# Kernel tuning notes

Measured on AMD Instinct MI355X. Metric: run time of the kernel, lower is better.

Reference implementation:

```python
import jax, jax.numpy as jnp
import numpy as np

N0, N1, N2 = 100000, 20000, 4000   # nodes per hierarchy level
F, H, C = 128, 128, 10             # num_features, hidden_dim, num_classes
E0, E1, E2 = 1600000, 320000, 64000  # intra-level edges (avg degree 16)
EPS = 1e-5                          # BatchNorm eps


def setup_inputs() -> dict:
    key = jax.random.key(0)
    ks = jax.random.split(key, 16)
    s = 0.05
    return {
        "x": jax.random.normal(ks[0], (N0, F), jnp.float32),
        "ei0": jax.random.randint(ks[1], (2, E0), 0, N0),
        "ei1": jax.random.randint(ks[2], (2, E1), 0, N1),
        "ei2": jax.random.randint(ks[3], (2, E2), 0, N2),
        "parent1": jax.random.randint(ks[4], (N0,), 0, N1),
        "parent2": jax.random.randint(ks[5], (N1,), 0, N2),
        "W0": jax.random.normal(ks[6], (F, H), jnp.float32) * s,
        "b0": jnp.zeros((H,), jnp.float32),
        "W1": jax.random.normal(ks[7], (H, H), jnp.float32) * s,
        "b1": jnp.zeros((H,), jnp.float32),
        "W2": jax.random.normal(ks[8], (H, H), jnp.float32) * s,
        "b2": jnp.zeros((H,), jnp.float32),
        "W3": jax.random.normal(ks[9], (2 * H, H), jnp.float32) * s,
        "b3": jnp.zeros((H,), jnp.float32),
        "W4": jax.random.normal(ks[10], (2 * H, C), jnp.float32) * s,
        "b4": jnp.zeros((C,), jnp.float32),
        "pW": jax.random.normal(ks[11], (4, H, H), jnp.float32) * s,
        "pb": jnp.zeros((4, H), jnp.float32),
        "pgamma": jnp.ones((4, H), jnp.float32),
        "pbeta": jnp.zeros((4, H), jnp.float32),
        "pmean": jax.random.normal(ks[12], (4, H), jnp.float32) * 0.1,
        "pvar": jax.random.uniform(ks[13], (4, H), jnp.float32, 0.5, 1.5),
    }


def _gcn(x, ei, W, b):
    # GCNConv: add self loops, symmetric D^-1/2 (A+I) D^-1/2 normalization.
    n = x.shape[0]
    loops = jnp.arange(n)
    row = jnp.concatenate([ei[0], loops])  # source nodes
    col = jnp.concatenate([ei[1], loops])  # target nodes
    deg = jax.ops.segment_sum(jnp.ones(row.shape, x.dtype), col, num_segments=n)
    dis = deg ** -0.5  # deg >= 1 because of self loops
    norm = dis[row] * dis[col]
    xw = x @ W
    out = jax.ops.segment_sum(norm[:, None] * xw[row], col, num_segments=n)
    return out + b


def _pool_nn(y, W, b, g, beta, mean, var):
    # SEPooling nn: Linear -> ReLU -> BatchNorm1d (eval mode, running stats)
    y = jax.nn.relu(y @ W + b)
    return (y - mean) * (g / jnp.sqrt(var + EPS)) + beta


def reference(x, ei0, ei1, ei2, parent1, parent2,
              W0, b0, W1, b1, W2, b2, W3, b3, W4, b4,
              pW, pb, pgamma, pbeta, pmean, pvar):
    relu = jax.nn.relu
    # down path (dropout is identity in eval mode)
    h0 = relu(_gcn(x, ei0, W0, b0))  # [N0,H]; stored skip xs[0]
    p = jax.ops.segment_sum(h0, parent1, num_segments=N1)  # scatter-add children -> parents
    x1 = relu(_pool_nn(p, pW[0], pb[0], pgamma[0], pbeta[0], pmean[0], pvar[0]))
    h1 = relu(_gcn(x1, ei1, W1, b1))  # [N1,H]; stored skip xs[1]
    p = jax.ops.segment_sum(h1, parent2, num_segments=N2)
    x2 = relu(_pool_nn(p, pW[1], pb[1], pgamma[1], pbeta[1], pmean[1], pvar[1]))
    # up path: conv, unpool (gather parent feature per child), concat skip
    h = relu(_gcn(x2, ei2, W2, b2))  # [N2,H]
    xu = relu(_pool_nn(h[parent2], pW[2], pb[2], pgamma[2], pbeta[2], pmean[2], pvar[2]))  # [N1,H]
    xc = jnp.concatenate([xu, h1], axis=1)  # [N1,2H]
    h = relu(_gcn(xc, ei1, W3, b3))  # [N1,H]
    xu = relu(_pool_nn(h[parent1], pW[3], pb[3], pgamma[3], pbeta[3], pmean[3], pvar[3]))  # [N0,H]
    xc = jnp.concatenate([xu, h0], axis=1)  # [N0,2H]
    out = _gcn(xc, ei0, W4, b4)  # [N0,C]
    return jax.nn.log_softmax(out, axis=-1)
```

## Files before the change

kernel.cpp:

```cpp
#include <hip/hip_runtime.h>
#include <math.h>

#define N0 100000
#define N1 20000
#define N2 4000
#define HDIM 128
#define E0C 1600000
#define E1C 320000
#define E2C 64000
#define EPSBN 1e-5f

typedef unsigned int u32;
typedef float f32x4 __attribute__((ext_vector_type(4)));
typedef short bf16x8 __attribute__((ext_vector_type(8)));

union FragU { uint4 u; bf16x8 h; };
__device__ __forceinline__ bf16x8 asbf(uint4 v) { FragU x; x.u = v; return x.h; }

__device__ __forceinline__ float bl(u32 p) { return __uint_as_float(p << 16); }
__device__ __forceinline__ float bh(u32 p) { return __uint_as_float(p & 0xFFFF0000u); }
__device__ __forceinline__ u32 pack2(float a, float b) {
    u32 ua = __float_as_uint(a), ub = __float_as_uint(b);
    ua = (ua + 0x7FFFu + ((ua >> 16) & 1u)) >> 16;
    ub = (ub + 0x7FFFu + ((ub >> 16) & 1u)) >> 16;
    return ua | (ub << 16);
}

#define OFF0 0
#define OFF1 (N0)
#define OFF2 (N0 + N1)
#define OFF3 (N0 + N1 + N2)
#define OFF4 (N0 + N1 + N2 + N1)
#define OFFT (N0 + N1 + N2 + N1 + N2)

#define S0 (E0C)
#define S1 (E0C + E1C)
#define S2 (E0C + E1C + E2C)
#define S3 (E0C + E1C + E2C + N0)
#define S4 (E0C + E1C + E2C + N0 + N1)

#define NBUCK ((OFFT + 1023) / 1024)
#define ITEMS_PER_BLK 2048
#define NBA ((S4 + ITEMS_PER_BLK - 1) / ITEMS_PER_BLK)
#define BH_N (NBUCK * NBA)
#define NBLK2 ((BH_N + 1023) / 1024)

#define NWMAT 9


__device__ __forceinline__ void item_full(int g,
    const int* __restrict__ ei0r, const int* __restrict__ ei0c,
    const int* __restrict__ ei1r, const int* __restrict__ ei1c,
    const int* __restrict__ ei2r, const int* __restrict__ ei2c,
    const int* __restrict__ p1, const int* __restrict__ p2,
    int& concat, int& payload)
{
    if (g < S0)      { concat = ei0c[g];             payload = ei0r[g]; }
    else if (g < S1) { int i = g - S0; concat = OFF1 + ei1c[i]; payload = ei1r[i]; }
    else if (g < S2) { int i = g - S1; concat = OFF2 + ei2c[i]; payload = ei2r[i]; }
    else if (g < S3) { int i = g - S2; concat = OFF3 + p1[i];   payload = i; }
    else             { int i = g - S3; concat = OFF4 + p2[i];   payload = i; }
}

__device__ __forceinline__ int item_concat(int g,
    const int* __restrict__ ei0c, const int* __restrict__ ei1c, const int* __restrict__ ei2c,
    const int* __restrict__ p1, const int* __restrict__ p2)
{
    if (g < S0)      return ei0c[g];
    else if (g < S1) return OFF1 + ei1c[g - S0];
    else if (g < S2) return OFF2 + ei2c[g - S1];
    else if (g < S3) return OFF3 + p1[g - S2];
    else             return OFF4 + p2[g - S3];
}

__global__ __launch_bounds__(256) void binhist_kernel(
    const int* __restrict__ ei0c, const int* __restrict__ ei1c, const int* __restrict__ ei2c,
    const int* __restrict__ p1, const int* __restrict__ p2,
    int* __restrict__ blockHist,
    const float* __restrict__ W0p, const float* __restrict__ W1p,
    const float* __restrict__ W2p, const float* __restrict__ W3p,
    const float* __restrict__ pWp, u32* __restrict__ Wpk)
{
    __shared__ int hist[NBUCK];
    int tid = threadIdx.x, blk = blockIdx.x;
    if (blk >= NBA) {
        int b = blk - NBA;
        const float* src;
        if (b == 0) src = W0p;
        else if (b == 1) src = W1p;
        else if (b == 2) src = W2p;
        else if (b == 3) src = W3p;
        else if (b == 4) src = W3p + 128 * 128;
        else src = pWp + (b - 5) * 128 * 128;
        u32* dst = Wpk + b * 8192;
        #pragma unroll
        for (int it = 0; it < 32; it++) {
            int flat = it * 256 + tid;
            int i = flat & 3;
            int ln = (flat >> 2) & 63;
            int s = (flat >> 8) & 3;
            int t = flat >> 10;
            int mm = ln & 15, qq = ln >> 4;
            int k0 = s * 32 + qq * 8 + 2 * i;
            int col = t * 16 + mm;
            dst[flat] = pack2(src[k0 * 128 + col], src[(k0 + 1) * 128 + col]);
        }
        return;
    }
    for (int i = tid; i < NBUCK; i += 256) hist[i] = 0;
    __syncthreads();
    int base = blk * ITEMS_PER_BLK;
    #pragma unroll
    for (int k = 0; k < ITEMS_PER_BLK / 256; k++) {
        int g = base + k * 256 + tid;
        if (g < S4) {
            int c = item_concat(g, ei0c, ei1c, ei2c, p1, p2);
            atomicAdd(&hist[c >> 10], 1);
        }
    }
    __syncthreads();
    for (int b = tid; b < NBUCK; b += 256) blockHist[b * NBA + blk] = hist[b];
}

__global__ __launch_bounds__(256) void scan_k1(const int* __restrict__ c, int* __restrict__ bsum, int n) {
    int t = threadIdx.x;
    int base = blockIdx.x * 1024 + t * 4;
    int s = 0;
    #pragma unroll
    for (int j = 0; j < 4; j++) {
        int idx = base + j;
        if (idx < n) s += c[idx];
    }
    #pragma unroll
    for (int o = 32; o > 0; o >>= 1) s += __shfl_down(s, o, 64);
    __shared__ int ws[4];
    if ((t & 63) == 0) ws[t >> 6] = s;
    __syncthreads();
    if (t == 0) bsum[blockIdx.x] = ws[0] + ws[1] + ws[2] + ws[3];
}

__global__ __launch_bounds__(256) void scan_k2(int* __restrict__ bsum, int* __restrict__ totalOut, int nb,
    const float* __restrict__ g, const float* __restrict__ beta,
    const float* __restrict__ mean, const float* __restrict__ var,
    float* __restrict__ scale, float* __restrict__ shift)
{
    int t = threadIdx.x;
    #pragma unroll
    for (int j = 0; j < 2; j++) {
        int i = j * 256 + t;
        float s = g[i] * rsqrtf(var[i] + EPSBN);
        scale[i] = s;
        shift[i] = beta[i] - mean[i] * s;
    }
    int v = (t < nb) ? bsum[t] : 0;
    __shared__ int ts[256];
    ts[t] = v;
    __syncthreads();
    for (int o = 1; o < 256; o <<= 1) {
        int u = (t >= o) ? ts[t - o] : 0;
        __syncthreads();
        ts[t] += u;
        __syncthreads();
    }
    if (t < nb) bsum[t] = ts[t] - v;
    if (t == nb - 1) *totalOut = ts[t];
}

__global__ __launch_bounds__(256) void scan_k3(const int* __restrict__ c, const int* __restrict__ bsum,
                                               const int* __restrict__ total,
                                               int* __restrict__ S, int n) {
    int t = threadIdx.x;
    int base = blockIdx.x * 1024 + t * 4;
    int v[4];
    #pragma unroll
    for (int j = 0; j < 4; j++) v[j] = (base + j < n) ? c[base + j] : 0;
    int tsum = v[0] + v[1] + v[2] + v[3];
    __shared__ int ts[256];
    ts[t] = tsum;
    __syncthreads();
    for (int o = 1; o < 256; o <<= 1) {
        int u = (t >= o) ? ts[t - o] : 0;
        __syncthreads();
        ts[t] += u;
        __syncthreads();
    }
    int run = bsum[blockIdx.x] + ts[t] - tsum;
    #pragma unroll
    for (int j = 0; j < 4; j++) {
        if (base + j < n) { S[base + j] = run; run += v[j]; }
    }
    if (blockIdx.x == 0 && t == 0) S[n] = *total;
}

__global__ __launch_bounds__(256) void binfill_kernel(
    const int* __restrict__ ei0r, const int* __restrict__ ei0c,
    const int* __restrict__ ei1r, const int* __restrict__ ei1c,
    const int* __restrict__ ei2r, const int* __restrict__ ei2c,
    const int* __restrict__ p1, const int* __restrict__ p2,
    const int* __restrict__ OfsAbs, u32* __restrict__ binPair)
{
    __shared__ int cur[NBUCK];
    int tid = threadIdx.x, blk = blockIdx.x;
    for (int i = tid; i < NBUCK; i += 256) cur[i] = OfsAbs[i * NBA + blk];
    __syncthreads();
    int base = blk * ITEMS_PER_BLK;
    #pragma unroll
    for (int k = 0; k < ITEMS_PER_BLK / 256; k++) {
        int g = base + k * 256 + tid;
        if (g < S4) {
            int c, p;
            item_full(g, ei0r, ei0c, ei1r, ei1c, ei2r, ei2c, p1, p2, c, p);
            int pos = atomicAdd(&cur[c >> 10], 1);
            binPair[pos] = ((u32)(c & 1023) << 17) | (u32)p;
        }
    }
}

__global__ __launch_bounds__(1024) void bucket_build_kernel(
    const u32* __restrict__ binPair, const int* __restrict__ OfsAbs,
    int* __restrict__ rpAll, int* __restrict__ srcU,
    float* __restrict__ dis0, float* __restrict__ dis1, float* __restrict__ dis2)
{
    __shared__ int cnt_l[1024];
    __shared__ int rp_l[1024];
    __shared__ int wsum[16];
    int b = blockIdx.x, tid = threadIdx.x;
    int start = OfsAbs[b * NBA];
    int end = (b + 1 < NBUCK) ? OfsAbs[(b + 1) * NBA] : S4;
    int d0 = b << 10;
    int nd = OFFT - d0; if (nd > 1024) nd = 1024;

    cnt_l[tid] = 0;
    __syncthreads();
    for (int i = start + tid; i < end; i += 1024) {
        u32 e = binPair[i];
        atomicAdd(&cnt_l[e >> 17], 1);
    }
    __syncthreads();
    int v = cnt_l[tid];
    int lane = tid & 63, wv = tid >> 6;
    int s = v;
    #pragma unroll
    for (int o = 1; o < 64; o <<= 1) {
        int u = __shfl_up(s, o, 64);
        if (lane >= o) s += u;
    }
    if (lane == 63) wsum[wv] = s;
    __syncthreads();
    if (wv == 0) {
        int t2 = (lane < 16) ? wsum[lane] : 0;
        #pragma unroll
        for (int o = 1; o < 16; o <<= 1) {
            int u = __shfl_up(t2, o, 64);
            if (lane >= o) t2 += u;
        }
        if (lane < 16) wsum[lane] = t2;
    }
    __syncthreads();
    int incl = s + (wv ? wsum[wv - 1] : 0);
    rp_l[tid] = incl - v;
    __syncthreads();
    if (tid < nd) {
        int g = d0 + tid;
        rpAll[g] = start + rp_l[tid];
        float dv = rsqrtf((float)(v + 1));
        if (g < OFF1) dis0[g] = dv;
        else if (g < OFF2) dis1[g - OFF1] = dv;
        else if (g < OFF3) dis2[g - OFF2] = dv;
    }
    if (b == NBUCK - 1 && tid == 0) rpAll[OFFT] = S4;
    __syncthreads();
    for (int i = start + tid; i < end; i += 1024) {
        u32 e = binPair[i];
        int pos = start + atomicAdd(&rp_l[e >> 17], 1);
        srcU[pos] = (int)(e & 0x1FFFFu);
    }
}


#define G128_LOAD(sym, off) u32 sym = y[(long long)srcl[e + off] * 64 + lane]

__global__ __launch_bounds__(256) void gather128_kernel(
    const int* __restrict__ rp, const int* __restrict__ srcl,
    const u32* __restrict__ y, const float* __restrict__ dis,
    const float* __restrict__ bias, u32* __restrict__ h, int n)
{
    int wid = (int)((blockIdx.x * 256 + threadIdx.x) >> 6);
    int lane = threadIdx.x & 63;
    if (wid >= n) return;
    u32 self = y[(long long)wid * 64 + lane];
    float ax = bl(self), ay = bh(self);
    int e = rp[wid], e1 = rp[wid + 1];
    for (; e + 7 < e1; e += 8) {
        G128_LOAD(p0, 0); G128_LOAD(p1, 1); G128_LOAD(p2, 2); G128_LOAD(p3, 3);
        G128_LOAD(p4, 4); G128_LOAD(p5, 5); G128_LOAD(p6, 6); G128_LOAD(p7, 7);
        ax += ((bl(p0) + bl(p1)) + (bl(p2) + bl(p3))) + ((bl(p4) + bl(p5)) + (bl(p6) + bl(p7)));
        ay += ((bh(p0) + bh(p1)) + (bh(p2) + bh(p3))) + ((bh(p4) + bh(p5)) + (bh(p6) + bh(p7)));
    }
    if (e + 3 < e1) {
        G128_LOAD(p0, 0); G128_LOAD(p1, 1); G128_LOAD(p2, 2); G128_LOAD(p3, 3);
        ax += (bl(p0) + bl(p1)) + (bl(p2) + bl(p3));
        ay += (bh(p0) + bh(p1)) + (bh(p2) + bh(p3));
        e += 4;
    }
    if (e + 1 < e1) {
        G128_LOAD(p0, 0); G128_LOAD(p1, 1);
        ax += bl(p0) + bl(p1);
        ay += bh(p0) + bh(p1);
        e += 2;
    }
    if (e < e1) {
        G128_LOAD(p0, 0);
        ax += bl(p0); ay += bh(p0);
    }
    float d = dis[wid];
    float2 b = ((const float2*)bias)[lane];
    float r0 = fmaxf(fmaf(d, ax, b.x), 0.f);
    float r1 = fmaxf(fmaf(d, ay, b.y), 0.f);
    h[(long long)wid * 64 + lane] = pack2(r0, r1);
}

__global__ __launch_bounds__(256) void gather10_lsm_kernel(
    const int* __restrict__ rp, const int* __restrict__ srcl,
    const u32* __restrict__ y4, const float* __restrict__ dis,
    const float* __restrict__ bias, float* __restrict__ out, int n)
{
    int c = blockIdx.x * blockDim.x + threadIdx.x;
    if (c >= n) return;
    float acc[10];
    {
        long long base = (long long)c * 8;
        uint4 q = *(const uint4*)(y4 + base);
        u32 q4 = y4[base + 4];
        acc[0] = bl(q.x); acc[1] = bh(q.x);
        acc[2] = bl(q.y); acc[3] = bh(q.y);
        acc[4] = bl(q.z); acc[5] = bh(q.z);
        acc[6] = bl(q.w); acc[7] = bh(q.w);
        acc[8] = bl(q4);  acc[9] = bh(q4);
    }
    int e = rp[c], e1 = rp[c + 1];
    for (; e + 3 < e1; e += 4) {
        long long bA = (long long)srcl[e] * 8;
        long long bB = (long long)srcl[e + 1] * 8;
        long long bC = (long long)srcl[e + 2] * 8;
        long long bD = (long long)srcl[e + 3] * 8;
        uint4 qa = *(const uint4*)(y4 + bA); u32 qa4 = y4[bA + 4];
        uint4 qb = *(const uint4*)(y4 + bB); u32 qb4 = y4[bB + 4];
        uint4 qc = *(const uint4*)(y4 + bC); u32 qc4 = y4[bC + 4];
        uint4 qd = *(const uint4*)(y4 + bD); u32 qd4 = y4[bD + 4];
        acc[0] += (bl(qa.x) + bl(qb.x)) + (bl(qc.x) + bl(qd.x));
        acc[1] += (bh(qa.x) + bh(qb.x)) + (bh(qc.x) + bh(qd.x));
        acc[2] += (bl(qa.y) + bl(qb.y)) + (bl(qc.y) + bl(qd.y));
        acc[3] += (bh(qa.y) + bh(qb.y)) + (bh(qc.y) + bh(qd.y));
        acc[4] += (bl(qa.z) + bl(qb.z)) + (bl(qc.z) + bl(qd.z));
        acc[5] += (bh(qa.z) + bh(qb.z)) + (bh(qc.z) + bh(qd.z));
        acc[6] += (bl(qa.w) + bl(qb.w)) + (bl(qc.w) + bl(qd.w));
        acc[7] += (bh(qa.w) + bh(qb.w)) + (bh(qc.w) + bh(qd.w));
        acc[8] += (bl(qa4) + bl(qb4)) + (bl(qc4) + bl(qd4));
        acc[9] += (bh(qa4) + bh(qb4)) + (bh(qc4) + bh(qd4));
    }
    for (; e < e1; e++) {
        long long bA = (long long)srcl[e] * 8;
        uint4 qa = *(const uint4*)(y4 + bA);
        u32 qa4 = y4[bA + 4];
        acc[0] += bl(qa.x); acc[1] += bh(qa.x);
        acc[2] += bl(qa.y); acc[3] += bh(qa.y);
        acc[4] += bl(qa.z); acc[5] += bh(qa.z);
        acc[6] += bl(qa.w); acc[7] += bh(qa.w);
        acc[8] += bl(qa4);  acc[9] += bh(qa4);
    }
    float d = dis[c];
    float m = -1e30f;
    #pragma unroll
    for (int k = 0; k < 10; k++) {
        acc[k] = fmaf(d, acc[k], bias[k]);
        m = fmaxf(m, acc[k]);
    }
    float s = 0.f;
    #pragma unroll
    for (int k = 0; k < 10; k++) s += expf(acc[k] - m);
    float ls = logf(s);
    #pragma unroll
    for (int k = 0; k < 10; k++) out[(long long)c * 10 + k] = acc[k] - m - ls;
}

__global__ __launch_bounds__(256) void mm128_kernel(
    const void* __restrict__ Av, const u32* __restrict__ Wp,
    u32* __restrict__ out, int M,
    const float* __restrict__ dis,
    const u32* __restrict__ gsrc, const int* __restrict__ gidx,
    const float* __restrict__ bias,
    const float* __restrict__ bnscale, const float* __restrict__ bnshift,
    int pool, int afp32,
    const int* __restrict__ pp, const int* __restrict__ childl, int apool)
{
    __shared__ u32 WL[8192];
    int tid = threadIdx.x;
    {
        const uint4* ws4 = (const uint4*)Wp;
        uint4* wd4 = (uint4*)WL;
        #pragma unroll
        for (int it = 0; it < 8; it++) wd4[it * 256 + tid] = ws4[it * 256 + tid];
    }
    __syncthreads();

    int lane = tid & 63;
    int w = tid >> 6;
    int m = lane & 15, q = lane >> 4;
    int row = blockIdx.x * 64 + w * 16 + m;
    bool live = (row < M);

    uint4 xb[4];
    if (live) {
        if (apool) {
            float fa[32];
            #pragma unroll
            for (int i = 0; i < 32; i++) fa[i] = 0.f;
            const u32* Hb = (const u32*)Av;
            int e = pp[row], eE = pp[row + 1];
            for (; e < eE; e++) {
                long long cb = (long long)childl[e] * 64;
                #pragma unroll
                for (int s = 0; s < 4; s++) {
                    uint4 vv = *(const uint4*)(Hb + cb + s * 16 + q * 4);
                    fa[s * 8 + 0] += bl(vv.x); fa[s * 8 + 1] += bh(vv.x);
                    fa[s * 8 + 2] += bl(vv.y); fa[s * 8 + 3] += bh(vv.y);
                    fa[s * 8 + 4] += bl(vv.z); fa[s * 8 + 5] += bh(vv.z);
                    fa[s * 8 + 6] += bl(vv.w); fa[s * 8 + 7] += bh(vv.w);
                }
            }
            #pragma unroll
            for (int s = 0; s < 4; s++) {
                xb[s].x = pack2(fa[s * 8 + 0], fa[s * 8 + 1]);
                xb[s].y = pack2(fa[s * 8 + 2], fa[s * 8 + 3]);
                xb[s].z = pack2(fa[s * 8 + 4], fa[s * 8 + 5]);
                xb[s].w = pack2(fa[s * 8 + 6], fa[s * 8 + 7]);
            }
        } else if (afp32) {
            const float* Af = (const float*)Av;
            #pragma unroll
            for (int s = 0; s < 4; s++) {
                const float4* p = (const float4*)(Af + (long long)row * 128 + s * 32 + q * 8);
                float4 f0 = p[0], f1 = p[1];
                xb[s].x = pack2(f0.x, f0.y);
                xb[s].y = pack2(f0.z, f0.w);
                xb[s].z = pack2(f1.x, f1.y);
                xb[s].w = pack2(f1.z, f1.w);
            }
        } else {
            const u32* Ab = (const u32*)Av;
            #pragma unroll
            for (int s = 0; s < 4; s++)
                xb[s] = *(const uint4*)(Ab + (long long)row * 64 + s * 16 + q * 4);
        }
    } else {
        xb[0] = xb[1] = xb[2] = xb[3] = make_uint4(0u, 0u, 0u, 0u);
    }

    float d = 1.0f;
    if (dis && live) d = dis[row];
    long long gbase = (gsrc && live) ? (long long)gidx[row] * 64 : 0;

    #pragma unroll
    for (int t = 0; t < 8; t++) {
        f32x4 acc = {0.f, 0.f, 0.f, 0.f};
        #pragma unroll
        for (int s = 0; s < 4; s++) {
            uint4 wa = *(const uint4*)&WL[((t * 4 + s) * 64 + lane) * 4];
            acc = __builtin_amdgcn_mfma_f32_16x16x32_bf16(asbf(wa), asbf(xb[s]), acc, 0, 0, 0);
        }
        if (live) {
            float v0 = acc[0], v1 = acc[1], v2 = acc[2], v3 = acc[3];
            int cbase = t * 16 + q * 4;
            if (gsrc) {
                uint2 g = *(const uint2*)(gsrc + gbase + (cbase >> 1));
                v0 += bl(g.x); v1 += bh(g.x);
                v2 += bl(g.y); v3 += bh(g.y);
            }
            if (pool) {
                float4 bb = *(const float4*)(bias + cbase);
                float4 sc = *(const float4*)(bnscale + cbase);
                float4 sh = *(const float4*)(bnshift + cbase);
                v0 = fmaxf(fmaxf(v0 + bb.x, 0.f) * sc.x + sh.x, 0.f);
                v1 = fmaxf(fmaxf(v1 + bb.y, 0.f) * sc.y + sh.y, 0.f);
                v2 = fmaxf(fmaxf(v2 + bb.z, 0.f) * sc.z + sh.z, 0.f);
                v3 = fmaxf(fmaxf(v3 + bb.w, 0.f) * sc.w + sh.w, 0.f);
            }
            v0 *= d; v1 *= d; v2 *= d; v3 *= d;
            uint2 st;
            st.x = pack2(v0, v1);
            st.y = pack2(v2, v3);
            *(uint2*)(out + (long long)row * 64 + (cbase >> 1)) = st;
        }
    }
}

#define TLP 68
__global__ __launch_bounds__(256) void mm128x2_kernel(
    const u32* __restrict__ Av, const u32* __restrict__ Wa, const u32* __restrict__ Wb,
    u32* __restrict__ out, int M,
    const float* __restrict__ dis2,
    const float* __restrict__ bias1,
    const float* __restrict__ bnscale1, const float* __restrict__ bnshift1,
    const int* __restrict__ pp, const int* __restrict__ childl, int apool,
    const float* __restrict__ W10, float* __restrict__ T0out, int Mt0)
{
    __shared__ u32 WL[8192];
    __shared__ u32 TL[64 * TLP];
    int tid = threadIdx.x;
    int nmm = (M + 63) >> 6;
    if ((int)blockIdx.x >= nmm) {
        int rowt = ((int)blockIdx.x - nmm) * 256 + tid;
        if (rowt < Mt0) {
            const uint4* a = (const uint4*)(Av + (long long)rowt * 64);
            float acc[10] = {0, 0, 0, 0, 0, 0, 0, 0, 0, 0};
            #pragma unroll 4
            for (int i = 0; i < 16; i++) {
                uint4 av = a[i];
                int k = i * 8;
                float f[8] = { bl(av.x), bh(av.x), bl(av.y), bh(av.y),
                               bl(av.z), bh(av.z), bl(av.w), bh(av.w) };
                #pragma unroll
                for (int j = 0; j < 8; j++) {
                    #pragma unroll
                    for (int cc = 0; cc < 10; cc++)
                        acc[cc] += f[j] * W10[(k + j) * 10 + cc];
                }
            }
            #pragma unroll
            for (int cc = 0; cc < 10; cc++) T0out[(long long)rowt * 10 + cc] = acc[cc];
        }
        return;
    }
    {
        const uint4* ws4 = (const uint4*)Wa;
        uint4* wd4 = (uint4*)WL;
        #pragma unroll
        for (int it = 0; it < 8; it++) wd4[it * 256 + tid] = ws4[it * 256 + tid];
    }
    __syncthreads();

    int lane = tid & 63;
    int w = tid >> 6;
    int m = lane & 15, q = lane >> 4;
    int row = blockIdx.x * 64 + w * 16 + m;
    bool live = (row < M);

    uint4 xb[4];
    if (live) {
        if (apool) {
            float fa[32];
            #pragma unroll
            for (int i = 0; i < 32; i++) fa[i] = 0.f;
            int e = pp[row], eE = pp[row + 1];
            for (; e < eE; e++) {
                long long cb = (long long)childl[e] * 64;
                #pragma unroll
                for (int s = 0; s < 4; s++) {
                    uint4 vv = *(const uint4*)(Av + cb + s * 16 + q * 4);
                    fa[s * 8 + 0] += bl(vv.x); fa[s * 8 + 1] += bh(vv.x);
                    fa[s * 8 + 2] += bl(vv.y); fa[s * 8 + 3] += bh(vv.y);
                    fa[s * 8 + 4] += bl(vv.z); fa[s * 8 + 5] += bh(vv.z);
                    fa[s * 8 + 6] += bl(vv.w); fa[s * 8 + 7] += bh(vv.w);
                }
            }
            #pragma unroll
            for (int s = 0; s < 4; s++) {
                xb[s].x = pack2(fa[s * 8 + 0], fa[s * 8 + 1]);
                xb[s].y = pack2(fa[s * 8 + 2], fa[s * 8 + 3]);
                xb[s].z = pack2(fa[s * 8 + 4], fa[s * 8 + 5]);
                xb[s].w = pack2(fa[s * 8 + 6], fa[s * 8 + 7]);
            }
        } else {
            #pragma unroll
            for (int s = 0; s < 4; s++)
                xb[s] = *(const uint4*)(Av + (long long)row * 64 + s * 16 + q * 4);
        }
    } else {
        xb[0] = xb[1] = xb[2] = xb[3] = make_uint4(0u, 0u, 0u, 0u);
    }

    u32* tl = TL + (w * 16 + m) * TLP;

    #pragma unroll
    for (int t = 0; t < 8; t++) {
        f32x4 acc = {0.f, 0.f, 0.f, 0.f};
        #pragma unroll
        for (int s = 0; s < 4; s++) {
            uint4 wa4 = *(const uint4*)&WL[((t * 4 + s) * 64 + lane) * 4];
            acc = __builtin_amdgcn_mfma_f32_16x16x32_bf16(asbf(wa4), asbf(xb[s]), acc, 0, 0, 0);
        }
        int cbase = t * 16 + q * 4;
        float4 bb = *(const float4*)(bias1 + cbase);
        float4 sc = *(const float4*)(bnscale1 + cbase);
        float4 sh = *(const float4*)(bnshift1 + cbase);
        float v0 = fmaxf(fmaxf(acc[0] + bb.x, 0.f) * sc.x + sh.x, 0.f);
        float v1 = fmaxf(fmaxf(acc[1] + bb.y, 0.f) * sc.y + sh.y, 0.f);
        float v2 = fmaxf(fmaxf(acc[2] + bb.z, 0.f) * sc.z + sh.z, 0.f);
        float v3 = fmaxf(fmaxf(acc[3] + bb.w, 0.f) * sc.w + sh.w, 0.f);
        uint2 st;
        st.x = pack2(v0, v1);
        st.y = pack2(v2, v3);
        *(uint2*)&tl[t * 8 + q * 2] = st;
    }
    __syncthreads();
    {
        const uint4* ws4 = (const uint4*)Wb;
        uint4* wd4 = (uint4*)WL;
        #pragma unroll
        for (int it = 0; it < 8; it++) wd4[it * 256 + tid] = ws4[it * 256 + tid];
    }
    __syncthreads();

    #pragma unroll
    for (int s = 0; s < 4; s++)
        xb[s] = *(const uint4*)&tl[s * 16 + q * 4];
    float d = 1.0f;
    if (dis2 && live) d = dis2[row];

    #pragma unroll
    for (int t = 0; t < 8; t++) {
        f32x4 acc = {0.f, 0.f, 0.f, 0.f};
        #pragma unroll
        for (int s = 0; s < 4; s++) {
            uint4 wa4 = *(const uint4*)&WL[((t * 4 + s) * 64 + lane) * 4];
            acc = __builtin_amdgcn_mfma_f32_16x16x32_bf16(asbf(wa4), asbf(xb[s]), acc, 0, 0, 0);
        }
        if (live) {
            int cbase = t * 16 + q * 4;
            float v0 = acc[0] * d, v1 = acc[1] * d, v2 = acc[2] * d, v3 = acc[3] * d;
            uint2 st;
            st.x = pack2(v0, v1);
            st.y = pack2(v2, v3);
            *(uint2*)(out + (long long)row * 64 + (cbase >> 1)) = st;
        }
    }
}

__global__ __launch_bounds__(256) void mm128_mm10_kernel(
    const u32* __restrict__ Av, const u32* __restrict__ Wp,
    const float* __restrict__ W10,
    float* __restrict__ out10, int M,
    const float* __restrict__ bias1,
    const float* __restrict__ bnscale1, const float* __restrict__ bnshift1)
{
    __shared__ u32 WL[8192];
    __shared__ u32 TL[64 * TLP];
    __shared__ float Ws[128 * 10];
    int tid = threadIdx.x;
    {
        const uint4* ws4 = (const uint4*)Wp;
        uint4* wd4 = (uint4*)WL;
        #pragma unroll
        for (int it = 0; it < 8; it++) wd4[it * 256 + tid] = ws4[it * 256 + tid];
    }
    for (int i = tid; i < 1280; i += 256) Ws[i] = W10[i];
    __syncthreads();

    int lane = tid & 63;
    int w = tid >> 6;
    int m = lane & 15, q = lane >> 4;
    int row = blockIdx.x * 64 + w * 16 + m;
    bool live = (row < M);

    uint4 xb[4];
    if (live) {
        #pragma unroll
        for (int s = 0; s < 4; s++)
            xb[s] = *(const uint4*)(Av + (long long)row * 64 + s * 16 + q * 4);
    } else {
        xb[0] = xb[1] = xb[2] = xb[3] = make_uint4(0u, 0u, 0u, 0u);
    }

    u32* tl = TL + (w * 16 + m) * TLP;

    #pragma unroll
    for (int t = 0; t < 8; t++) {
        f32x4 acc = {0.f, 0.f, 0.f, 0.f};
        #pragma unroll
        for (int s = 0; s < 4; s++) {
            uint4 wa4 = *(const uint4*)&WL[((t * 4 + s) * 64 + lane) * 4];
            acc = __builtin_amdgcn_mfma_f32_16x16x32_bf16(asbf(wa4), asbf(xb[s]), acc, 0, 0, 0);
        }
        int cbase = t * 16 + q * 4;
        float4 bb = *(const float4*)(bias1 + cbase);
        float4 sc = *(const float4*)(bnscale1 + cbase);
        float4 sh = *(const float4*)(bnshift1 + cbase);
        float v0 = fmaxf(fmaxf(acc[0] + bb.x, 0.f) * sc.x + sh.x, 0.f);
        float v1 = fmaxf(fmaxf(acc[1] + bb.y, 0.f) * sc.y + sh.y, 0.f);
        float v2 = fmaxf(fmaxf(acc[2] + bb.z, 0.f) * sc.z + sh.z, 0.f);
        float v3 = fmaxf(fmaxf(acc[3] + bb.w, 0.f) * sc.w + sh.w, 0.f);
        uint2 st;
        st.x = pack2(v0, v1);
        st.y = pack2(v2, v3);
        *(uint2*)&tl[t * 8 + q * 2] = st;
    }
    __syncthreads();

    int base = blockIdx.x * 64;
    for (int slot = tid; slot < 640; slot += 256) {
        int r = slot / 10, cc = slot % 10;
        if (base + r < M) {
            const u32* tr = &TL[r * TLP];
            float acc = 0.f;
            #pragma unroll
            for (int k2 = 0; k2 < 64; k2++) {
                u32 p = tr[k2];
                acc += bl(p) * Ws[(2 * k2) * 10 + cc];
                acc += bh(p) * Ws[(2 * k2 + 1) * 10 + cc];
            }
            out10[(long long)(base + r) * 10 + cc] = acc;
        }
    }
}

__global__ __launch_bounds__(256) void mm10p2_kernel(
    const float* __restrict__ T0, const float* __restrict__ gsrc,
    const int* __restrict__ gidx, const float* __restrict__ dis,
    u32* __restrict__ outp, int M)
{
    int row = blockIdx.x * 256 + threadIdx.x;
    if (row >= M) return;
    float d = dis[row];
    const float* t = T0 + (long long)row * 10;
    const float* g = gsrc + (long long)gidx[row] * 10;
    long long base = (long long)row * 8;
    #pragma unroll
    for (int j = 0; j < 5; j++) {
        float v0 = (t[2 * j] + g[2 * j]) * d;
        float v1 = (t[2 * j + 1] + g[2 * j + 1]) * d;
        outp[base + j] = pack2(v0, v1);
    }
}


extern "C" void kernel_launch(void* const* d_in, const int* in_sizes, int n_in,
                              void* d_out, int out_size, void* d_ws, size_t ws_size,
                              hipStream_t stream) {
    const float* x       = (const float*)d_in[0];
    const int*   ei0     = (const int*)d_in[1];
    const int*   ei1     = (const int*)d_in[2];
    const int*   ei2     = (const int*)d_in[3];
    const int*   parent1 = (const int*)d_in[4];
    const int*   parent2 = (const int*)d_in[5];
    const float* W0 = (const float*)d_in[6];
    const float* b0 = (const float*)d_in[7];
    const float* W1 = (const float*)d_in[8];
    const float* b1 = (const float*)d_in[9];
    const float* W2 = (const float*)d_in[10];
    const float* b2 = (const float*)d_in[11];
    const float* W3 = (const float*)d_in[12];
    const float* b3 = (const float*)d_in[13];
    const float* W4 = (const float*)d_in[14];
    const float* b4 = (const float*)d_in[15];
    const float* pW = (const float*)d_in[16];
    const float* pb = (const float*)d_in[17];
    const float* pg = (const float*)d_in[18];
    const float* pbeta = (const float*)d_in[19];
    const float* pmean = (const float*)d_in[20];
    const float* pvar  = (const float*)d_in[21];
    float* out = (float*)d_out;

    char* ws = (char*)d_ws;
    size_t off = 0;
    auto alloc = [&](size_t nbytes) -> char* {
        char* p = ws + off;
        off += ((nbytes + 255) / 256) * 256;
        return p;
    };
    float* dis0 = (float*)alloc(N0 * 4);
    float* dis1 = (float*)alloc(N1 * 4);
    float* dis2 = (float*)alloc(N2 * 4);
    float* bnscale = (float*)alloc(4 * HDIM * 4);
    float* bnshift = (float*)alloc(4 * HDIM * 4);
    float* W1b = (float*)alloc((size_t)N1 * 10 * 4);
    float* T0  = (float*)alloc((size_t)N0 * 10 * 4);
    u32* Y   = (u32*)alloc((size_t)N0 * 64 * 4);
    u32* H0  = (u32*)alloc((size_t)N0 * 64 * 4);
    u32* H1  = (u32*)alloc((size_t)N1 * 64 * 4);
    u32* HU1 = (u32*)alloc((size_t)N1 * 64 * 4);
    u32* H2  = (u32*)alloc((size_t)N2 * 64 * 4);
    u32* V2  = (u32*)alloc((size_t)N2 * 64 * 4);
    u32* Y4p = (u32*)alloc((size_t)N0 * 8 * 4);
    u32* Wpk = (u32*)alloc((size_t)NWMAT * 8192 * 4);
    int* rpAll = (int*)alloc((size_t)(OFFT + 1) * 4);
    int* srcU  = (int*)alloc((size_t)S4 * 4);
    int* blockHist = (int*)alloc((size_t)BH_N * 4);
    int* OfsAbs    = (int*)alloc((size_t)(BH_N + 1) * 4);
    u32* binPair   = (u32*)alloc((size_t)S4 * 4);
    int* bsum   = (int*)alloc(NBLK2 * 4);
    int* totalb = (int*)alloc(4);

    const int B = 256;
    auto G = [](long long t) { return (unsigned)((t + 255) / 256); };
    auto G64 = [](long long m) { return (unsigned)((m + 63) / 64); };

    binhist_kernel<<<NBA + NWMAT, B, 0, stream>>>(
        ei0 + E0C, ei1 + E1C, ei2 + E2C, parent1, parent2, blockHist,
        W0, W1, W2, W3, pW, Wpk);
    scan_k1<<<NBLK2, B, 0, stream>>>(blockHist, bsum, BH_N);
    scan_k2<<<1, B, 0, stream>>>(bsum, totalb, NBLK2, pg, pbeta, pmean, pvar, bnscale, bnshift);
    scan_k3<<<NBLK2, B, 0, stream>>>(blockHist, bsum, totalb, OfsAbs, BH_N);
    binfill_kernel<<<NBA, B, 0, stream>>>(
        ei0, ei0 + E0C, ei1, ei1 + E1C, ei2, ei2 + E2C, parent1, parent2, OfsAbs, binPair);
    bucket_build_kernel<<<NBUCK, 1024, 0, stream>>>(
        binPair, OfsAbs, rpAll, srcU, dis0, dis1, dis2);

    mm128_kernel<<<G64(N0), B, 0, stream>>>(
        x, Wpk + 0 * 8192, Y, N0, dis0, nullptr, nullptr, nullptr, nullptr, nullptr, 0, 1,
        nullptr, nullptr, 0);
    gather128_kernel<<<G((long long)N0 * 64), B, 0, stream>>>(rpAll + OFF0, srcU, Y, dis0, b0, H0, N0);

    mm128x2_kernel<<<G64(N1) + G(N0), B, 0, stream>>>(
        H0, Wpk + 5 * 8192, Wpk + 1 * 8192, Y, N1, dis1,
        pb, bnscale, bnshift, rpAll + OFF3, srcU, 1,
        W4 + 128 * 10, T0, N0);
    gather128_kernel<<<G((long long)N1 * 64), B, 0, stream>>>(rpAll + OFF1, srcU, Y, dis1, b1, H1, N1);

    mm128x2_kernel<<<G64(N2), B, 0, stream>>>(
        H1, Wpk + 6 * 8192, Wpk + 2 * 8192, Y, N2, dis2,
        pb + 128, bnscale + 128, bnshift + 128, rpAll + OFF4, srcU, 1,
        nullptr, nullptr, 0);
    gather128_kernel<<<G((long long)N2 * 64), B, 0, stream>>>(rpAll + OFF2, srcU, Y, dis2, b2, H2, N2);

    mm128x2_kernel<<<G64(N2), B, 0, stream>>>(
        H2, Wpk + 7 * 8192, Wpk + 3 * 8192, V2, N2, nullptr,
        pb + 256, bnscale + 256, bnshift + 256, nullptr, nullptr, 0,
        nullptr, nullptr, 0);

    mm128_kernel<<<G64(N1), B, 0, stream>>>(
        H1, Wpk + 4 * 8192, Y, N1, dis1, V2, parent2, nullptr, nullptr, nullptr, 0, 0,
        nullptr, nullptr, 0);
    gather128_kernel<<<G((long long)N1 * 64), B, 0, stream>>>(rpAll + OFF1, srcU, Y, dis1, b3, HU1, N1);

    mm128_mm10_kernel<<<G64(N1), B, 0, stream>>>(
        HU1, Wpk + 8 * 8192, W4, W1b, N1, pb + 384, bnscale + 384, bnshift + 384);

    mm10p2_kernel<<<G(N0), B, 0, stream>>>(T0, W1b, parent1, dis0, Y4p, N0);
    gather10_lsm_kernel<<<G(N0), B, 0, stream>>>(rpAll + OFF0, srcU, Y4p, dis0, b4, out, N0);
}
```

Baseline: 377.1 us.

## Split level-0 GCN gather into two column-half passes over a half-split layout

```diff
diff --git a/kernel.cpp b/kernel.cpp
--- a/kernel.cpp
+++ b/kernel.cpp
@@ -277,6 +277,57 @@
     }
 }
 
+
+__global__ __launch_bounds__(256) void gather128h_kernel(
+    const int* __restrict__ rp, const int* __restrict__ srcl,
+    const u32* __restrict__ yh, const float* __restrict__ dis,
+    const float* __restrict__ biasHalf, u32* __restrict__ hHalf, int n)
+{
+    int wid = (int)((blockIdx.x * 256 + threadIdx.x) >> 6);
+    int lane = threadIdx.x & 63;
+    if (wid >= n) return;
+    int l32 = lane & 31;
+    int epar = lane >> 5;
+    u32 self = yh[(long long)wid * 32 + l32];
+    float ax = (epar == 0) ? bl(self) : 0.f;
+    float ay = (epar == 0) ? bh(self) : 0.f;
+    int e0 = rp[wid], e1 = rp[wid + 1];
+    int eb = e0;
+    for (; eb + 7 < e1; eb += 8) {
+        int i0 = eb + epar;
+        int s0 = srcl[i0], s1 = srcl[i0 + 2], s2 = srcl[i0 + 4], s3 = srcl[i0 + 6];
+        u32 p0 = yh[(long long)s0 * 32 + l32];
+        u32 p1 = yh[(long long)s1 * 32 + l32];
+        u32 p2 = yh[(long long)s2 * 32 + l32];
+        u32 p3 = yh[(long long)s3 * 32 + l32];
+        ax += (bl(p0) + bl(p1)) + (bl(p2) + bl(p3));
+        ay += (bh(p0) + bh(p1)) + (bh(p2) + bh(p3));
+    }
+    for (; eb + 3 < e1; eb += 4) {
+        int i0 = eb + epar;
+        int s0 = srcl[i0], s1 = srcl[i0 + 2];
+        u32 p0 = yh[(long long)s0 * 32 + l32];
+        u32 p1 = yh[(long long)s1 * 32 + l32];
+        ax += bl(p0) + bl(p1);
+        ay += bh(p0) + bh(p1);
+    }
+    for (; eb < e1; eb += 2) {
+        int ei = eb + epar;
+        bool v = ei < e1;
+        int si = v ? srcl[ei] : wid;
+        u32 p = yh[(long long)si * 32 + l32];
+        if (v) { ax += bl(p); ay += bh(p); }
+    }
+    ax += __shfl_xor(ax, 32, 64);
+    ay += __shfl_xor(ay, 32, 64);
+    if (epar == 0) {
+        float d = dis[wid];
+        float2 b = ((const float2*)biasHalf)[l32];
+        float r0 = fmaxf(fmaf(d, ax, b.x), 0.f);
+        float r1 = fmaxf(fmaf(d, ay, b.y), 0.f);
+        hHalf[(long long)wid * 64 + l32] = pack2(r0, r1);
+    }
+}
 
 #define G128_LOAD(sym, off) u32 sym = y[(long long)srcl[e + off] * 64 + lane]
 
@@ -392,7 +443,8 @@
     const float* __restrict__ bias,
     const float* __restrict__ bnscale, const float* __restrict__ bnshift,
     int pool, int afp32,
-    const int* __restrict__ pp, const int* __restrict__ childl, int apool)
+    const int* __restrict__ pp, const int* __restrict__ childl, int apool,
+    int halfout)
 {
     __shared__ u32 WL[8192];
     int tid = threadIdx.x;
@@ -490,7 +542,10 @@
             uint2 st;
             st.x = pack2(v0, v1);
             st.y = pack2(v2, v3);
-            *(uint2*)(out + (long long)row * 64 + (cbase >> 1)) = st;
+            if (halfout)
+                *(uint2*)(out + ((long long)(t >> 2) * M + row) * 32 + (t & 3) * 8 + q * 2) = st;
+            else
+                *(uint2*)(out + (long long)row * 64 + (cbase >> 1)) = st;
         }
     }
 }
@@ -808,8 +863,11 @@
 
     mm128_kernel<<<G64(N0), B, 0, stream>>>(
         x, Wpk + 0 * 8192, Y, N0, dis0, nullptr, nullptr, nullptr, nullptr, nullptr, 0, 1,
-        nullptr, nullptr, 0);
-    gather128_kernel<<<G((long long)N0 * 64), B, 0, stream>>>(rpAll + OFF0, srcU, Y, dis0, b0, H0, N0);
+        nullptr, nullptr, 0, 1);
+    gather128h_kernel<<<G((long long)N0 * 64), B, 0, stream>>>(
+        rpAll + OFF0, srcU, Y, dis0, b0, H0, N0);
+    gather128h_kernel<<<G((long long)N0 * 64), B, 0, stream>>>(
+        rpAll + OFF0, srcU, Y + (long long)N0 * 32, dis0, b0 + 64, H0 + 32, N0);
 
     mm128x2_kernel<<<G64(N1) + G(N0), B, 0, stream>>>(
         H0, Wpk + 5 * 8192, Wpk + 1 * 8192, Y, N1, dis1,
@@ -830,7 +888,7 @@
 
     mm128_kernel<<<G64(N1), B, 0, stream>>>(
         H1, Wpk + 4 * 8192, Y, N1, dis1, V2, parent2, nullptr, nullptr, nullptr, 0, 0,
-        nullptr, nullptr, 0);
+        nullptr, nullptr, 0, 0);
     gather128_kernel<<<G((long long)N1 * 64), B, 0, stream>>>(rpAll + OFF1, srcU, Y, dis1, b3, HU1, N1);
 
     mm128_mm10_kernel<<<G64(N1), B, 0, stream>>>(
```

Measured after the change: 422.4 us. 12.0% more time.

## Compute degrees early via global atomics and fuse first matmul into binfill

Applied to the files above, without the earlier changes.

```diff
diff --git a/kernel.cpp b/kernel.cpp
--- a/kernel.cpp
+++ b/kernel.cpp
@@ -46,6 +46,8 @@
 #define NBLK2 ((BH_N + 1023) / 1024)
 
 #define NWMAT 9
+#define G64N0 ((N0 + 63) / 64)
+#define DISB ((OFF3 + 255) / 256)
 
 
 __device__ __forceinline__ void item_full(int g,
@@ -76,7 +78,7 @@
 __global__ __launch_bounds__(256) void binhist_kernel(
     const int* __restrict__ ei0c, const int* __restrict__ ei1c, const int* __restrict__ ei2c,
     const int* __restrict__ p1, const int* __restrict__ p2,
-    int* __restrict__ blockHist,
+    int* __restrict__ blockHist, int* __restrict__ deg,
     const float* __restrict__ W0p, const float* __restrict__ W1p,
     const float* __restrict__ W2p, const float* __restrict__ W3p,
     const float* __restrict__ pWp, u32* __restrict__ Wpk)
@@ -116,14 +118,28 @@
         if (g < S4) {
             int c = item_concat(g, ei0c, ei1c, ei2c, p1, p2);
             atomicAdd(&hist[c >> 10], 1);
+            atomicAdd(&deg[c], 1);
         }
     }
     __syncthreads();
     for (int b = tid; b < NBUCK; b += 256) blockHist[b * NBA + blk] = hist[b];
 }
 
-__global__ __launch_bounds__(256) void scan_k1(const int* __restrict__ c, int* __restrict__ bsum, int n) {
+__global__ __launch_bounds__(256) void scan_k1(const int* __restrict__ c, int* __restrict__ bsum, int n,
+    const int* __restrict__ deg,
+    float* __restrict__ dis0, float* __restrict__ dis1, float* __restrict__ dis2)
+{
     int t = threadIdx.x;
+    if ((int)blockIdx.x >= NBLK2) {
+        int g = ((int)blockIdx.x - NBLK2) * 256 + t;
+        if (g < OFF3) {
+            float dv = rsqrtf((float)(deg[g] + 1));
+            if (g < OFF1) dis0[g] = dv;
+            else if (g < OFF2) dis1[g - OFF1] = dv;
+            else dis2[g - OFF2] = dv;
+        }
+        return;
+    }
     int base = blockIdx.x * 1024 + t * 4;
     int s = 0;
     #pragma unroll
@@ -197,10 +213,53 @@
     const int* __restrict__ ei1r, const int* __restrict__ ei1c,
     const int* __restrict__ ei2r, const int* __restrict__ ei2c,
     const int* __restrict__ p1, const int* __restrict__ p2,
-    const int* __restrict__ OfsAbs, u32* __restrict__ binPair)
+    const int* __restrict__ OfsAbs, u32* __restrict__ binPair,
+    const float* __restrict__ xin, const u32* __restrict__ Wpk0,
+    const float* __restrict__ dis0, u32* __restrict__ Yout)
 {
     __shared__ int cur[NBUCK];
     int tid = threadIdx.x, blk = blockIdx.x;
+    if (blk >= NBA) {
+        int bb = blk - NBA;
+        int lane = tid & 63;
+        int w = tid >> 6;
+        int m = lane & 15, q = lane >> 4;
+        int row = bb * 64 + w * 16 + m;
+        bool live = (row < N0);
+        uint4 xb[4];
+        if (live) {
+            #pragma unroll
+            for (int s = 0; s < 4; s++) {
+                const float4* p = (const float4*)(xin + (long long)row * 128 + s * 32 + q * 8);
+                float4 f0 = p[0], f1 = p[1];
+                xb[s].x = pack2(f0.x, f0.y);
+                xb[s].y = pack2(f0.z, f0.w);
+                xb[s].z = pack2(f1.x, f1.y);
+                xb[s].w = pack2(f1.z, f1.w);
+            }
+        } else {
+            xb[0] = xb[1] = xb[2] = xb[3] = make_uint4(0u, 0u, 0u, 0u);
+        }
+        float d = live ? dis0[row] : 1.0f;
+        #pragma unroll
+        for (int t = 0; t < 8; t++) {
+            f32x4 acc = {0.f, 0.f, 0.f, 0.f};
+            #pragma unroll
+            for (int s = 0; s < 4; s++) {
+                uint4 wa = *(const uint4*)&Wpk0[((t * 4 + s) * 64 + lane) * 4];
+                acc = __builtin_amdgcn_mfma_f32_16x16x32_bf16(asbf(wa), asbf(xb[s]), acc, 0, 0, 0);
+            }
+            if (live) {
+                float v0 = acc[0] * d, v1 = acc[1] * d, v2 = acc[2] * d, v3 = acc[3] * d;
+                int cbase = t * 16 + q * 4;
+                uint2 st;
+                st.x = pack2(v0, v1);
+                st.y = pack2(v2, v3);
+                *(uint2*)(Yout + (long long)row * 64 + (cbase >> 1)) = st;
+            }
+        }
+        return;
+    }
     for (int i = tid; i < NBUCK; i += 256) cur[i] = OfsAbs[i * NBA + blk];
     __syncthreads();
     int base = blk * ITEMS_PER_BLK;
@@ -218,8 +277,7 @@
 
 __global__ __launch_bounds__(1024) void bucket_build_kernel(
     const u32* __restrict__ binPair, const int* __restrict__ OfsAbs,
-    int* __restrict__ rpAll, int* __restrict__ srcU,
-    float* __restrict__ dis0, float* __restrict__ dis1, float* __restrict__ dis2)
+    int* __restrict__ rpAll, int* __restrict__ srcU)
 {
     __shared__ int cnt_l[1024];
     __shared__ int rp_l[1024];
@@ -260,14 +318,7 @@
     int incl = s + (wv ? wsum[wv - 1] : 0);
     rp_l[tid] = incl - v;
     __syncthreads();
-    if (tid < nd) {
-        int g = d0 + tid;
-        rpAll[g] = start + rp_l[tid];
-        float dv = rsqrtf((float)(v + 1));
-        if (g < OFF1) dis0[g] = dv;
-        else if (g < OFF2) dis1[g - OFF1] = dv;
-        else if (g < OFF3) dis2[g - OFF2] = dv;
-    }
+    if (tid < nd) rpAll[d0 + tid] = start + rp_l[tid];
     if (b == NBUCK - 1 && tid == 0) rpAll[OFFT] = S4;
     __syncthreads();
     for (int i = start + tid; i < end; i += 1024) {
@@ -790,25 +841,24 @@
     u32* binPair   = (u32*)alloc((size_t)S4 * 4);
     int* bsum   = (int*)alloc(NBLK2 * 4);
     int* totalb = (int*)alloc(4);
+    int* deg    = (int*)alloc((size_t)OFFT * 4);
 
     const int B = 256;
     auto G = [](long long t) { return (unsigned)((t + 255) / 256); };
     auto G64 = [](long long m) { return (unsigned)((m + 63) / 64); };
 
+    hipMemsetAsync(deg, 0, (size_t)OFFT * 4, stream);
     binhist_kernel<<<NBA + NWMAT, B, 0, stream>>>(
-        ei0 + E0C, ei1 + E1C, ei2 + E2C, parent1, parent2, blockHist,
+        ei0 + E0C, ei1 + E1C, ei2 + E2C, parent1, parent2, blockHist, deg,
         W0, W1, W2, W3, pW, Wpk);
-    scan_k1<<<NBLK2, B, 0, stream>>>(blockHist, bsum, BH_N);
+    scan_k1<<<NBLK2 + DISB, B, 0, stream>>>(blockHist, bsum, BH_N, deg, dis0, dis1, dis2);
     scan_k2<<<1, B, 0, stream>>>(bsum, totalb, NBLK2, pg, pbeta, pmean, pvar, bnscale, bnshift);
     scan_k3<<<NBLK2, B, 0, stream>>>(blockHist, bsum, totalb, OfsAbs, BH_N);
-    binfill_kernel<<<NBA, B, 0, stream>>>(
-        ei0, ei0 + E0C, ei1, ei1 + E1C, ei2, ei2 + E2C, parent1, parent2, OfsAbs, binPair);
-    bucket_build_kernel<<<NBUCK, 1024, 0, stream>>>(
-        binPair, OfsAbs, rpAll, srcU, dis0, dis1, dis2);
-
-    mm128_kernel<<<G64(N0), B, 0, stream>>>(
-        x, Wpk + 0 * 8192, Y, N0, dis0, nullptr, nullptr, nullptr, nullptr, nullptr, 0, 1,
-        nullptr, nullptr, 0);
+    binfill_kernel<<<NBA + G64N0, B, 0, stream>>>(
+        ei0, ei0 + E0C, ei1, ei1 + E1C, ei2, ei2 + E2C, parent1, parent2, OfsAbs, binPair,
+        x, Wpk + 0 * 8192, dis0, Y);
+    bucket_build_kernel<<<NBUCK, 1024, 0, stream>>>(binPair, OfsAbs, rpAll, srcU);
+
     gather128_kernel<<<G((long long)N0 * 64), B, 0, stream>>>(rpAll + OFF0, srcU, Y, dis0, b0, H0, N0);
 
     mm128x2_kernel<<<G64(N1) + G(N0), B, 0, stream>>>(
```

After: 466.1 us. 23.6% more time.
